# Optimization experiments

Measured on AMD Instinct MI355X. Metric: run time of the kernel, lower is better.

## Reference

```python
import jax, jax.numpy as jnp
import numpy as np

NUM_HEAD = 16
SIZE_PER_HEAD = 64
D_MODEL = NUM_HEAD * SIZE_PER_HEAD
BATCH = 4
SEQ = 2048
MASK_VAL = 1e10  # module uses 10000000000.0 for the causal mask


def setup_inputs() -> dict:
    key = jax.random.key(0)
    ks = jax.random.split(key, 11)
    s = 1.0 / np.sqrt(D_MODEL)
    return {
        "q": jax.random.normal(ks[0], (BATCH, SEQ, D_MODEL), jnp.float32),
        "k": jax.random.normal(ks[1], (BATCH, SEQ, D_MODEL), jnp.float32),
        "v": jax.random.normal(ks[2], (BATCH, SEQ, D_MODEL), jnp.float32),
        "WQ": jax.random.normal(ks[3], (D_MODEL, D_MODEL), jnp.float32) * s,
        "WQ_bias": jax.random.normal(ks[4], (D_MODEL,), jnp.float32) * 0.02,
        "WK": jax.random.normal(ks[5], (D_MODEL, D_MODEL), jnp.float32) * s,
        "WK_bias": jax.random.normal(ks[6], (D_MODEL,), jnp.float32) * 0.02,
        "WV": jax.random.normal(ks[7], (D_MODEL, D_MODEL), jnp.float32) * s,
        "WV_bias": jax.random.normal(ks[8], (D_MODEL,), jnp.float32) * 0.02,
        "WO": jax.random.normal(ks[9], (D_MODEL, D_MODEL), jnp.float32) * s,
        "WO_bias": jax.random.normal(ks[10], (D_MODEL,), jnp.float32) * 0.02,
    }


def _split_heads(x):
    # [B, S, H*D] -> [B, H, S, D]
    b, s, _ = x.shape
    return x.reshape(b, s, NUM_HEAD, SIZE_PER_HEAD).transpose(0, 2, 1, 3)


def reference(q, k, v, WQ, WQ_bias, WK, WK_bias, WV, WV_bias, WO, WO_bias):
    Q = _split_heads(q @ WQ + WQ_bias)  # [B,H,M,D]
    Kh = _split_heads(k @ WK + WK_bias)  # [B,H,N,D]
    Vh = _split_heads(v @ WV + WV_bias)  # [B,H,N,D]

    A = jnp.einsum('bhmd,bhnd->bhmn', Q, Kh)
    # causal mask (is_right=True): subtract 1e10 on strict upper triangle,
    # applied BEFORE the 1/sqrt(d) scale, exactly as the original.
    m, n = A.shape[-2], A.shape[-1]
    causal = jnp.triu(jnp.ones((m, n), A.dtype), k=1) * jnp.asarray(MASK_VAL, A.dtype)
    A = A - causal
    A = jax.nn.softmax(A / np.sqrt(SIZE_PER_HEAD).astype(np.float32), axis=-1)

    O = jnp.einsum('bhmn,bhnd->bhmd', A, Vh)  # [B,H,M,D]
    b, h, s, d = O.shape
    O = O.transpose(0, 2, 1, 3).reshape(b, s, h * d)
    return O @ WO + WO_bias
```

## Files before the change

### kernel.cpp

```cpp
#include <hip/hip_runtime.h>
#include <hip/hip_bf16.h>

typedef unsigned short u16;
typedef __attribute__((ext_vector_type(8))) short bf8_t;
typedef __attribute__((ext_vector_type(4))) float f4_t;
typedef __attribute__((ext_vector_type(2))) unsigned u32x2_t;
typedef __attribute__((ext_vector_type(4))) unsigned u32x4_t;

#define D_MODEL 1024
#define SEQ     2048
#define NHEAD   16
#define DH      64
#define MTOK    8192
#define ELEMS_PER_MAT 8388608

__device__ __forceinline__ u16 f2b(float x) {
    unsigned u = __float_as_uint(x);
    u += 0x7fffu + ((u >> 16) & 1u);
    return (u16)(u >> 16);
}

__device__ __forceinline__ unsigned pkrn(float lo, float hi) {
    __hip_bfloat162 h = __float22bfloat162_rn(make_float2(lo, hi));
    unsigned r;
    __builtin_memcpy(&r, &h, 4);
    return r;
}

__device__ __forceinline__ float ex2(float x) {
    float r;
    asm("v_exp_f32 %0, %1" : "=v"(r) : "v"(x));
    return r;
}

__device__ __forceinline__ void gl_lds16(const void* g, void* l) {
    __builtin_amdgcn_global_load_lds(
        (const __attribute__((address_space(1))) void*)g,
        (__attribute__((address_space(3))) void*)l, 16, 0, 0);
}

struct P3 { const float* p[3]; };

#define QSCALE 0.1803368801111244f
struct W4 { const float* w[4]; };
__global__ void cvt_wt(W4 wa, u16* __restrict__ wt) {
    int z = blockIdx.z;
    const float* W = wa.w[z];
    u16* Wt = wt + (size_t)z * 1048576;
    float scale = (z == 0) ? QSCALE : 1.0f;
    __shared__ float tl[64][65];
    int t = threadIdx.x;
    int bx = blockIdx.x, by = blockIdx.y;
#pragma unroll
    for (int i = 0; i < 16; i++) {
        int e = i * 256 + t;
        int row = e >> 6, col = e & 63;
        tl[row][col] = W[(size_t)(by * 64 + row) * 1024 + bx * 64 + col];
    }
    __syncthreads();
#pragma unroll
    for (int i = 0; i < 16; i++) {
        int e = i * 256 + t;
        int row = e >> 6, col = e & 63;
        Wt[(size_t)(bx * 64 + row) * 1024 + by * 64 + col] = f2b(tl[col][row] * scale);
    }
}

struct B4 { const float* b[4]; };
__global__ void cvt_bias(B4 ba, float* __restrict__ dst) {
    int t = threadIdx.x;
    for (int z = 0; z < 4; z++) {
        float sc = (z == 0) ? QSCALE : 1.0f;
        for (int i = t; i < 1024; i += 256) dst[z * 1024 + i] = ba.b[z][i] * sc;
    }
}

template <int MODE>
__global__ __launch_bounds__(256, 2) void gemm_k(P3 a3,
                                                 const u16* __restrict__ Ab16,
                                                 const u16* __restrict__ Btb,
                                                 const float* __restrict__ biasb,
                                                 void* __restrict__ out0,
                                                 u16* __restrict__ outV) {
    int z = blockIdx.z;
    const float* Af = (MODE == 3) ? a3.p[z] : nullptr;
    const u16* Bt = Btb + (size_t)z * 1048576;
    const float* bias = biasb + z * 1024;
    bool vswap = (MODE == 3) && (z == 2);

    int bid = blockIdx.y * 64 + blockIdx.x;
    int xcd = bid & 7, seq = bid >> 3;
    int tm = xcd * 8 + (seq & 7);
    int tn = seq >> 3;
    int t = threadIdx.x;
    int wid = t >> 6, lane = t & 63;
    int wm = wid >> 1, wn = wid & 1;
    int la = lane & 15, lh = lane >> 4;

    __shared__ __align__(16) char smem[65536];

    f4_t acc[4][4];
#pragma unroll
    for (int m = 0; m < 4; m++)
#pragma unroll
        for (int n = 0; n < 4; n++) acc[m][n] = (f4_t){0.f, 0.f, 0.f, 0.f};

    const u16* Bgb = Bt + (size_t)(tn * 128) * 1024;

    int ch0 = wid * 64 + lane;
    int so0 = (lh ^ (la & 7)) * 8;
    int so1 = so0 ^ 32;

    f4_t areg[4][2];

    auto aload = [&](int k0) {
#pragma unroll
        for (int i = 0; i < 4; i++) {
            int ch = ch0 + i * 256;
            int row = ch >> 3, c8 = ch & 7;
            const float* src = Af + (size_t)(tm * 128 + row) * 1024 + k0 + c8 * 8;
            areg[i][0] = *(const f4_t*)src;
            areg[i][1] = *(const f4_t*)(src + 4);
        }
    };
    auto awrite = [&](int b) {
#pragma unroll
        for (int i = 0; i < 4; i++) {
            int ch = ch0 + i * 256;
            int row = ch >> 3, c8 = ch & 7;
            int slot = c8 ^ (row & 7);
            u32x4_t w;
            w[0] = pkrn(areg[i][0][0], areg[i][0][1]);
            w[1] = pkrn(areg[i][0][2], areg[i][0][3]);
            w[2] = pkrn(areg[i][1][0], areg[i][1][1]);
            w[3] = pkrn(areg[i][1][2], areg[i][1][3]);
            *(u32x4_t*)(smem + b * 32768 + (row * 8 + slot) * 16) = w;
        }
    };
    auto astage16 = [&](int k0, int b) {
        const u16* Agb = Ab16 + (size_t)(tm * 128) * 1024;
#pragma unroll
        for (int i = 0; i < 4; i++) {
            int ch = ch0 + i * 256;
            int row = ch >> 3, c8 = ch & 7;
            int srcc = (c8 ^ (row & 7)) * 8;
            gl_lds16(Agb + (size_t)row * 1024 + k0 + srcc,
                     smem + b * 32768 + (size_t)(i * 4 + wid) * 1024);
        }
    };
    auto bstage = [&](int k0, int b) {
#pragma unroll
        for (int i = 0; i < 4; i++) {
            int ch = ch0 + i * 256;
            int row = ch >> 3, c8 = ch & 7;
            int srcc = (c8 ^ (row & 7)) * 8;
            gl_lds16(Bgb + (size_t)row * 1024 + k0 + srcc,
                     smem + b * 32768 + 16384 + (size_t)(i * 4 + wid) * 1024);
        }
    };

    if (MODE == 3) { aload(0); bstage(0, 0); awrite(0); }
    else           { astage16(0, 0); bstage(0, 0); }
    __syncthreads();

    int cur = 0;
    for (int kt = 0; kt < 16; kt++) {
        if (kt + 1 < 16) {
            if (MODE == 3) { aload((kt + 1) * 64); bstage((kt + 1) * 64, cur ^ 1); }
            else { astage16((kt + 1) * 64, cur ^ 1); bstage((kt + 1) * 64, cur ^ 1); }
        }
        const u16* As = (const u16*)(smem + cur * 32768);
        const u16* Bs = (const u16*)(smem + cur * 32768 + 16384);
#pragma unroll
        for (int ks = 0; ks < 2; ks++) {
            int so = ks ? so1 : so0;
            bf8_t af[4], bf[4];
#pragma unroll
            for (int m = 0; m < 4; m++)
                af[m] = *(const bf8_t*)&As[(wm * 64 + m * 16 + la) * 64 + so];
#pragma unroll
            for (int n = 0; n < 4; n++)
                bf[n] = *(const bf8_t*)&Bs[(wn * 64 + n * 16 + la) * 64 + so];
            if (vswap) {
#pragma unroll
                for (int m = 0; m < 4; m++)
#pragma unroll
                    for (int n = 0; n < 4; n++)
                        acc[m][n] = __builtin_amdgcn_mfma_f32_16x16x32_bf16(bf[n], af[m], acc[m][n], 0, 0, 0);
            } else {
#pragma unroll
                for (int m = 0; m < 4; m++)
#pragma unroll
                    for (int n = 0; n < 4; n++)
                        acc[m][n] = __builtin_amdgcn_mfma_f32_16x16x32_bf16(af[m], bf[n], acc[m][n], 0, 0, 0);
            }
        }
        if (MODE == 3 && kt + 1 < 16) awrite(cur ^ 1);
        __syncthreads();
        cur ^= 1;
    }

    int lh4 = lh * 4;
    int bq = tm >> 4;
    int sloc = (tm & 15) * 128;

    if (MODE == 1) {
        float* ef = (float*)smem;
#pragma unroll
        for (int m = 0; m < 4; m++) {
            int row = wm * 64 + m * 16 + lh4;
#pragma unroll
            for (int n = 0; n < 4; n++) {
                int cb = wn * 64 + n * 16;
                float bv = bias[tn * 128 + cb + la];
#pragma unroll
                for (int r = 0; r < 4; r++)
                    ef[(row + r) * 128 + cb + la] = acc[m][n][r] + bv;
            }
        }
        __syncthreads();
        float* og = (float*)out0;
#pragma unroll
        for (int p = 0; p < 16; p++) {
            int e = t * 4 + p * 1024;
            int row = e >> 7, col = e & 127;
            f4_t v = *(const f4_t*)&ef[e];
            *(f4_t*)&og[(size_t)(tm * 128 + row) * 1024 + tn * 128 + col] = v;
        }
    } else if (vswap) {
        u16* eb = (u16*)smem;
#pragma unroll
        for (int m = 0; m < 4; m++) {
            int s = wm * 64 + m * 16 + la;
#pragma unroll
            for (int n = 0; n < 4; n++) {
                int cb = wn * 64 + n * 16 + lh4;
#pragma unroll
                for (int r = 0; r < 4; r++)
                    eb[(cb + r) * 128 + s] = f2b(acc[m][n][r] + bias[tn * 128 + cb + r]);
            }
        }
        __syncthreads();
#pragma unroll
        for (int p = 0; p < 8; p++) {
            int col = (t >> 4) + p * 16;
            int chunk = (t & 15) * 8;
            int h = tn * 2 + (col >> 6), d = col & 63;
            bf8_t v = *(const bf8_t*)&eb[col * 128 + chunk];
            *(bf8_t*)&outV[(((size_t)(bq * NHEAD + h)) * DH + d) * SEQ + sloc + chunk] = v;
        }
    } else {
        u16* eb = (u16*)smem;
#pragma unroll
        for (int m = 0; m < 4; m++) {
            int row = wm * 64 + m * 16 + lh4;
#pragma unroll
            for (int n = 0; n < 4; n++) {
                int cb = wn * 64 + n * 16;
                float bv = bias[tn * 128 + cb + la];
#pragma unroll
                for (int r = 0; r < 4; r++)
                    eb[wn * 8192 + (row + r) * 64 + n * 16 + la] = f2b(acc[m][n][r] + bv);
            }
        }
        __syncthreads();
        u16* outz = (u16*)out0 + (size_t)z * ELEMS_PER_MAT;
        size_t gbase = ((size_t)(bq * NHEAD + tn * 2) * SEQ + sloc) * DH;
#pragma unroll
        for (int p = 0; p < 8; p++) {
            int e = t * 8 + p * 2048;
            int hl = e >> 13, inner = e & 8191;
            bf8_t v = *(const bf8_t*)&eb[e];
            *(bf8_t*)&outz[gbase + (size_t)hl * SEQ * DH + inner] = v;
        }
    }
}

__global__ __launch_bounds__(256, 4) void attn(const u16* __restrict__ Qp,
                                               const u16* __restrict__ Kp,
                                               const u16* __restrict__ Vt,
                                               u16* __restrict__ ctx) {
    int id = blockIdx.x;
    int qt = 31 - (id >> 6);
    int bh = id & 63;
    int t = threadIdx.x, wid = t >> 6, lane = t & 63;
    int la = lane & 15, lh = lane >> 4;
    int lh4 = lh * 4;
    int lh8 = lh * 8;
    int q0 = qt * 64;

    const u16* Qb = Qp + (size_t)bh * SEQ * DH;
    const u16* Kb = Kp + (size_t)bh * SEQ * DH;
    const u16* Vb = Vt + (size_t)bh * DH * SEQ;

    __shared__ __align__(16) u16 Kl[2 * 4096];
    __shared__ __align__(16) u16 Vl[2 * 4096];

    int qrow = q0 + wid * 16 + la;
    bf8_t qf0 = *(const bf8_t*)&Qb[(size_t)qrow * DH + lh8];
    bf8_t qf1 = *(const bf8_t*)&Qb[(size_t)qrow * DH + 32 + lh8];

    bf8_t onesf;
#pragma unroll
    for (int i = 0; i < 8; i++) onesf[i] = (short)0x3F80;

    float m = -1e30f;
    f4_t o[4] = {};
    f4_t o5  = {};

    int s0 = t, s1 = t + 256;
    int rr0 = s0 >> 3, rr1 = s1 >> 3;
    int ck0 = ((s0 & 7) ^ (rr0 & 7)) * 8;
    int ck1 = ((s1 & 7) ^ (rr1 & 7)) * 8;
    int key0 = (rr0 & 0x23) | ((rr0 & 0x0C) << 1) | ((rr0 & 0x10) >> 2);
    int key1 = (rr1 & 0x23) | ((rr1 & 0x0C) << 1) | ((rr1 & 0x10) >> 2);
    const u16* kp0 = Kb + (size_t)key0 * DH + ck0;
    const u16* kp1 = Kb + (size_t)key1 * DH + ck1;
    const u16* vp0 = Vb + (size_t)rr0 * SEQ + ck0;
    const u16* vp1 = Vb + (size_t)rr1 * SEQ + ck1;

    int ntiles = qt + 1;
    auto stage = [&](int tile, int b) {
        int kv0 = tile * 64;
        gl_lds16(kp0 + (size_t)kv0 * DH, (char*)Kl + b * 8192 + wid * 1024);
        gl_lds16(kp1 + (size_t)kv0 * DH, (char*)Kl + b * 8192 + 4096 + wid * 1024);
        gl_lds16(vp0 + kv0,              (char*)Vl + b * 8192 + wid * 1024);
        gl_lds16(vp1 + kv0,              (char*)Vl + b * 8192 + 4096 + wid * 1024);
    };
    stage(0, 0);

    int csA = (lh ^ (la & 7)) * 8;
    int csB = ((4 | lh) ^ (la & 7)) * 8;

    for (int tkv = 0; tkv < ntiles; ++tkv) {
        __syncthreads();
        if (tkv + 1 < ntiles) stage(tkv + 1, (tkv + 1) & 1);
        const u16* Kd = Kl + (tkv & 1) * 4096;
        const u16* Vd = Vl + (tkv & 1) * 4096;

        bool diag = (tkv == qt);
        int ntmax = diag ? ((wid < 2) ? 2 : 4) : 4;

        f4_t st[4];
        __builtin_amdgcn_s_setprio(1);
#pragma unroll
        for (int nt = 0; nt < 4; nt++) {
            if (nt < ntmax) {
                bf8_t kf0 = *(const bf8_t*)&Kd[(nt * 16 + la) * 64 + csA];
                bf8_t kf1 = *(const bf8_t*)&Kd[(nt * 16 + la) * 64 + csB];
                f4_t a = (f4_t){0.f, 0.f, 0.f, 0.f};
                a = __builtin_amdgcn_mfma_f32_16x16x32_bf16(kf0, qf0, a, 0, 0, 0);
                a = __builtin_amdgcn_mfma_f32_16x16x32_bf16(kf1, qf1, a, 0, 0, 0);
                if (diag) {
                    int kbase = ((nt >> 1) << 5) + (lh << 3) + ((nt & 1) << 2);
#pragma unroll
                    for (int r = 0; r < 4; r++)
                        if (kbase + r > wid * 16 + la) a[r] = -1e30f;
                }
                st[nt] = a;
            } else {
                st[nt] = (f4_t){-1e30f, -1e30f, -1e30f, -1e30f};
            }
        }
        __builtin_amdgcn_s_setprio(0);

        float mloc = -3e38f;
#pragma unroll
        for (int nt = 0; nt < 4; nt++)
            if (nt < ntmax) {
                mloc = fmaxf(mloc, fmaxf(fmaxf(st[nt][0], st[nt][1]),
                                         fmaxf(st[nt][2], st[nt][3])));
            }
        mloc = fmaxf(mloc, __shfl_xor(mloc, 16));
        mloc = fmaxf(mloc, __shfl_xor(mloc, 32));
        if (!__all(mloc <= m + 8.0f)) {
            float mnew = fmaxf(m, mloc);
            float alpha = ex2(m - mnew);
#pragma unroll
            for (int dm = 0; dm < 4; dm++) o[dm] *= alpha;
            o5 *= alpha;
            m = mnew;
        }

#pragma unroll
        for (int nt = 0; nt < 4; nt++) {
#pragma unroll
            for (int r = 0; r < 4; r++)
                st[nt][r] = ex2(st[nt][r] - m);
        }

        __builtin_amdgcn_s_setprio(1);
#pragma unroll
        for (int kk = 0; kk < 2; kk++) {
            if (2 * kk < ntmax) {
                u32x4_t pw;
                pw[0] = pkrn(st[2 * kk][0], st[2 * kk][1]);
                pw[1] = pkrn(st[2 * kk][2], st[2 * kk][3]);
                pw[2] = pkrn(st[2 * kk + 1][0], st[2 * kk + 1][1]);
                pw[3] = pkrn(st[2 * kk + 1][2], st[2 * kk + 1][3]);
                bf8_t pf;
                __builtin_memcpy(&pf, &pw, 16);
                int cs = kk ? csB : csA;
#pragma unroll
                for (int dm = 0; dm < 4; dm++) {
                    bf8_t vf = *(const bf8_t*)&Vd[(dm * 16 + la) * 64 + cs];
                    o[dm] = __builtin_amdgcn_mfma_f32_16x16x32_bf16(vf, pf, o[dm], 0, 0, 0);
                }
                o5 = __builtin_amdgcn_mfma_f32_16x16x32_bf16(onesf, pf, o5, 0, 0, 0);
            }
        }
        __builtin_amdgcn_s_setprio(0);
    }

    float inv = 1.0f / o5[0];
    int b = bh >> 4, h = bh & 15;
    size_t base = ((size_t)(b * SEQ + qrow)) * D_MODEL + h * DH;
#pragma unroll
    for (int dm = 0; dm < 4; dm++) {
        u32x2_t w;
        w[0] = pkrn(o[dm][0] * inv, o[dm][1] * inv);
        w[1] = pkrn(o[dm][2] * inv, o[dm][3] * inv);
        *(u32x2_t*)&ctx[base + dm * 16 + lh4] = w;
    }
}

extern "C" void kernel_launch(void* const* d_in, const int* in_sizes, int n_in,
                              void* d_out, int out_size, void* d_ws, size_t ws_size,
                              hipStream_t stream) {
    const float* q   = (const float*)d_in[0];
    const float* k   = (const float*)d_in[1];
    const float* v   = (const float*)d_in[2];
    const float* WQ  = (const float*)d_in[3];
    const float* WQb = (const float*)d_in[4];
    const float* WK  = (const float*)d_in[5];
    const float* WKb = (const float*)d_in[6];
    const float* WV  = (const float*)d_in[7];
    const float* WVb = (const float*)d_in[8];
    const float* WO  = (const float*)d_in[9];
    const float* WOb = (const float*)d_in[10];

    char* ws = (char*)d_ws;
    u16*   Wt     = (u16*)(ws + 50331648);
    float* biasws = (float*)(ws + 58720256);
    u16*   QKVp   = (u16*)(ws + 58736640);
    u16*   Vt_    = (u16*)(ws + 109068288);
    u16*   ctx    = (u16*)(ws + 125845504);

    W4 w4; w4.w[0] = WQ; w4.w[1] = WK; w4.w[2] = WV; w4.w[3] = WO;
    cvt_wt<<<dim3(16, 16, 4), 256, 0, stream>>>(w4, Wt);
    B4 b4; b4.b[0] = WQb; b4.b[1] = WKb; b4.b[2] = WVb; b4.b[3] = WOb;
    cvt_bias<<<1, 256, 0, stream>>>(b4, biasws);

    P3 a3; a3.p[0] = q; a3.p[1] = k; a3.p[2] = v;
    gemm_k<3><<<dim3(64, 8, 3), 256, 0, stream>>>(a3, nullptr, Wt, biasws, QKVp, Vt_);

    attn<<<dim3(2048), 256, 0, stream>>>(QKVp, QKVp + ELEMS_PER_MAT, Vt_, ctx);

    P3 dummy; dummy.p[0] = dummy.p[1] = dummy.p[2] = nullptr;
    gemm_k<1><<<dim3(64, 8, 1), 256, 0, stream>>>(dummy, ctx, Wt + 3 * 1048576,
                                                  biasws + 3 * 1024, d_out, nullptr);
}
```

Baseline: 181.3 us.

## Deepen fp32 A-operand prefetch to two stages with explicit vmcnt waits

Result: slower. 243.1 us (+34.1%).

```diff
diff --git a/kernel.cpp b/kernel.cpp
--- a/kernel.cpp
+++ b/kernel.cpp
@@ -13,6 +13,11 @@
 #define DH      64
 #define MTOK    8192
 #define ELEMS_PER_MAT 8388608
+
+#define ASM_VMCNT(N) do { asm volatile("s_waitcnt vmcnt(" #N ")" ::: "memory"); \
+                          __builtin_amdgcn_sched_barrier(0); } while (0)
+#define ASM_LGKM0    do { asm volatile("s_waitcnt lgkmcnt(0)" ::: "memory");    \
+                          __builtin_amdgcn_sched_barrier(0); } while (0)
 
 __device__ __forceinline__ u16 f2b(float x) {
     unsigned u = __float_as_uint(x);
@@ -111,43 +116,6 @@
     int so0 = (lh ^ (la & 7)) * 8;
     int so1 = so0 ^ 32;
 
-    f4_t areg[4][2];
-
-    auto aload = [&](int k0) {
-#pragma unroll
-        for (int i = 0; i < 4; i++) {
-            int ch = ch0 + i * 256;
-            int row = ch >> 3, c8 = ch & 7;
-            const float* src = Af + (size_t)(tm * 128 + row) * 1024 + k0 + c8 * 8;
-            areg[i][0] = *(const f4_t*)src;
-            areg[i][1] = *(const f4_t*)(src + 4);
-        }
-    };
-    auto awrite = [&](int b) {
-#pragma unroll
-        for (int i = 0; i < 4; i++) {
-            int ch = ch0 + i * 256;
-            int row = ch >> 3, c8 = ch & 7;
-            int slot = c8 ^ (row & 7);
-            u32x4_t w;
-            w[0] = pkrn(areg[i][0][0], areg[i][0][1]);
-            w[1] = pkrn(areg[i][0][2], areg[i][0][3]);
-            w[2] = pkrn(areg[i][1][0], areg[i][1][1]);
-            w[3] = pkrn(areg[i][1][2], areg[i][1][3]);
-            *(u32x4_t*)(smem + b * 32768 + (row * 8 + slot) * 16) = w;
-        }
-    };
-    auto astage16 = [&](int k0, int b) {
-        const u16* Agb = Ab16 + (size_t)(tm * 128) * 1024;
-#pragma unroll
-        for (int i = 0; i < 4; i++) {
-            int ch = ch0 + i * 256;
-            int row = ch >> 3, c8 = ch & 7;
-            int srcc = (c8 ^ (row & 7)) * 8;
-            gl_lds16(Agb + (size_t)row * 1024 + k0 + srcc,
-                     smem + b * 32768 + (size_t)(i * 4 + wid) * 1024);
-        }
-    };
     auto bstage = [&](int k0, int b) {
 #pragma unroll
         for (int i = 0; i < 4; i++) {
@@ -159,18 +127,9 @@
         }
     };
 
-    if (MODE == 3) { aload(0); bstage(0, 0); awrite(0); }
-    else           { astage16(0, 0); bstage(0, 0); }
-    __syncthreads();
-
-    int cur = 0;
-    for (int kt = 0; kt < 16; kt++) {
-        if (kt + 1 < 16) {
-            if (MODE == 3) { aload((kt + 1) * 64); bstage((kt + 1) * 64, cur ^ 1); }
-            else { astage16((kt + 1) * 64, cur ^ 1); bstage((kt + 1) * 64, cur ^ 1); }
-        }
-        const u16* As = (const u16*)(smem + cur * 32768);
-        const u16* Bs = (const u16*)(smem + cur * 32768 + 16384);
+    auto compute = [&](int b) {
+        const u16* As = (const u16*)(smem + b * 32768);
+        const u16* Bs = (const u16*)(smem + b * 32768 + 16384);
 #pragma unroll
         for (int ks = 0; ks < 2; ks++) {
             int so = ks ? so1 : so0;
@@ -195,9 +154,116 @@
                         acc[m][n] = __builtin_amdgcn_mfma_f32_16x16x32_bf16(af[m], bf[n], acc[m][n], 0, 0, 0);
             }
         }
-        if (MODE == 3 && kt + 1 < 16) awrite(cur ^ 1);
+    };
+
+    if (MODE == 3) {
+        f4_t aregA[4][2], aregB[4][2];
+        auto aloadA = [&](int k0) {
+#pragma unroll
+            for (int i = 0; i < 4; i++) {
+                int ch = ch0 + i * 256;
+                int row = ch >> 3, c8 = ch & 7;
+                const float* src = Af + (size_t)(tm * 128 + row) * 1024 + k0 + c8 * 8;
+                aregA[i][0] = *(const f4_t*)src;
+                aregA[i][1] = *(const f4_t*)(src + 4);
+            }
+        };
+        auto aloadB = [&](int k0) {
+#pragma unroll
+            for (int i = 0; i < 4; i++) {
+                int ch = ch0 + i * 256;
+                int row = ch >> 3, c8 = ch & 7;
+                const float* src = Af + (size_t)(tm * 128 + row) * 1024 + k0 + c8 * 8;
+                aregB[i][0] = *(const f4_t*)src;
+                aregB[i][1] = *(const f4_t*)(src + 4);
+            }
+        };
+        auto awriteA = [&](int b) {
+#pragma unroll
+            for (int i = 0; i < 4; i++) {
+                int ch = ch0 + i * 256;
+                int row = ch >> 3, c8 = ch & 7;
+                int slot = c8 ^ (row & 7);
+                u32x4_t w;
+                w[0] = pkrn(aregA[i][0][0], aregA[i][0][1]);
+                w[1] = pkrn(aregA[i][0][2], aregA[i][0][3]);
+                w[2] = pkrn(aregA[i][1][0], aregA[i][1][1]);
+                w[3] = pkrn(aregA[i][1][2], aregA[i][1][3]);
+                *(u32x4_t*)(smem + b * 32768 + (row * 8 + slot) * 16) = w;
+            }
+        };
+        auto awriteB = [&](int b) {
+#pragma unroll
+            for (int i = 0; i < 4; i++) {
+                int ch = ch0 + i * 256;
+                int row = ch >> 3, c8 = ch & 7;
+                int slot = c8 ^ (row & 7);
+                u32x4_t w;
+                w[0] = pkrn(aregB[i][0][0], aregB[i][0][1]);
+                w[1] = pkrn(aregB[i][0][2], aregB[i][0][3]);
+                w[2] = pkrn(aregB[i][1][0], aregB[i][1][1]);
+                w[3] = pkrn(aregB[i][1][2], aregB[i][1][3]);
+                *(u32x4_t*)(smem + b * 32768 + (row * 8 + slot) * 16) = w;
+            }
+        };
+
+        aloadA(0);
+        aloadB(64);
+        bstage(0, 0);
+        awriteA(0);
+        ASM_LGKM0;
+        __builtin_amdgcn_s_barrier();
+
+        for (int kp = 0; kp < 8; kp++) {
+            if (kp < 7) {
+                aloadA((2 * kp + 2) * 64);
+                bstage((2 * kp + 1) * 64, 1);
+                ASM_VMCNT(12);
+            } else {
+                bstage((2 * kp + 1) * 64, 1);
+                ASM_VMCNT(4);
+            }
+            compute(0);
+            awriteB(1);
+            ASM_LGKM0;
+            __builtin_amdgcn_s_barrier();
+            if (kp < 7) {
+                aloadB((2 * kp + 3) * 64);
+                bstage((2 * kp + 2) * 64, 0);
+                ASM_VMCNT(12);
+            } else {
+                ASM_VMCNT(0);
+            }
+            compute(1);
+            if (kp < 7) awriteA(0);
+            ASM_LGKM0;
+            __builtin_amdgcn_s_barrier();
+        }
+    } else {
+        auto astage16 = [&](int k0, int b) {
+            const u16* Agb = Ab16 + (size_t)(tm * 128) * 1024;
+#pragma unroll
+            for (int i = 0; i < 4; i++) {
+                int ch = ch0 + i * 256;
+                int row = ch >> 3, c8 = ch & 7;
+                int srcc = (c8 ^ (row & 7)) * 8;
+                gl_lds16(Agb + (size_t)row * 1024 + k0 + srcc,
+                         smem + b * 32768 + (size_t)(i * 4 + wid) * 1024);
+            }
+        };
+        astage16(0, 0);
+        bstage(0, 0);
         __syncthreads();
-        cur ^= 1;
+        int cur = 0;
+        for (int kt = 0; kt < 16; kt++) {
+            if (kt + 1 < 16) {
+                astage16((kt + 1) * 64, cur ^ 1);
+                bstage((kt + 1) * 64, cur ^ 1);
+            }
+            compute(cur);
+            __syncthreads();
+            cur ^= 1;
+        }
     }
 
     int lh4 = lh * 4;
```
